# Kernel tuning notes

Measured on AMD Instinct MI355X. Metric: run time of the kernel, lower is better.

Reference implementation:

```python
import jax, jax.numpy as jnp
import numpy as np

B, S, D, H, E, K = 2, 1024, 768, 12, 8, 2
DF = 4 * D
HD = D // H
EPS = 1e-5

def layer_norm(x, g, b):
    m = jnp.mean(x, axis=-1, keepdims=True)
    v = jnp.mean(jnp.square(x - m), axis=-1, keepdims=True)
    return (x - m) * jax.lax.rsqrt(v + EPS) * g + b

def setup_inputs() -> dict:
    key = jax.random.key(0)
    ks = jax.random.split(key, 16)
    s = lambda i, shape, sc: jax.random.normal(ks[i], shape, jnp.float32) * sc
    return {
        'x': s(0, (B, S, D), 1.0),
        'ln1_g': jnp.ones((D,), jnp.float32), 'ln1_b': jnp.zeros((D,), jnp.float32),
        'Wq': s(1, (D, D), 0.02), 'Wk': s(2, (D, D), 0.02), 'Wv': s(3, (D, D), 0.02),
        'Wo': s(4, (D, D), 0.02), 'bo': jnp.zeros((D,), jnp.float32),
        'ln2_g': jnp.ones((D,), jnp.float32), 'ln2_b': jnp.zeros((D,), jnp.float32),
        'Wr': s(5, (D, E), 0.02), 'br': jnp.zeros((E,), jnp.float32),
        'W1': s(6, (E, D, DF), 0.02), 'b1': jnp.zeros((E, DF), jnp.float32),
        'W2': s(7, (E, DF, D), 0.02), 'b2': jnp.zeros((E, D), jnp.float32),
    }

def _attn(xn, Wq, Wk, Wv, Wo, bo):
    # xn: [B,S,D]
    q = (xn @ Wq).reshape(B, S, H, HD).transpose(0, 2, 1, 3)
    k = (xn @ Wk).reshape(B, S, H, HD).transpose(0, 2, 1, 3)
    v = (xn @ Wv).reshape(B, S, H, HD).transpose(0, 2, 1, 3)
    scores = jnp.einsum('bhqd,bhkd->bhqk', q, k) / jnp.sqrt(jnp.float32(HD))
    causal = jnp.tril(jnp.ones((S, S), bool))
    scores = jnp.where(causal, scores, jnp.float32(-1e9))
    w = jax.nn.softmax(scores, axis=-1)
    out = jnp.einsum('bhqk,bhkd->bhqd', w, v)
    out = out.transpose(0, 2, 1, 3).reshape(B, S, D)
    return out @ Wo + bo

def _smoe(xn, Wr, br, W1, b1, W2, b2):
    logits = xn @ Wr + br                               # [B,S,E]
    topv, topi = jax.lax.top_k(logits, K)               # [B,S,K]
    gw = jax.nn.softmax(topv, axis=-1)                  # softmax over selected experts
    oh = jax.nn.one_hot(topi, E, dtype=xn.dtype)        # [B,S,K,E]
    gate = jnp.einsum('bske,bsk->bse', oh, gw)          # sparse gate, zeros elsewhere
    h = jax.nn.gelu(jnp.einsum('bsd,edf->bsef', xn, W1) + b1, approximate=False)
    eo = jnp.einsum('bsef,efd->bsed', h, W2) + b2       # [B,S,E,D]
    return jnp.einsum('bsed,bse->bsd', eo, gate)

def reference(x, ln1_g, ln1_b, Wq, Wk, Wv, Wo, bo, ln2_g, ln2_b, Wr, br, W1, b1, W2, b2):
    h = x + _attn(layer_norm(x, ln1_g, ln1_b), Wq, Wk, Wv, Wo, bo)
    out = h + _smoe(layer_norm(h, ln2_g, ln2_b), Wr, br, W1, b1, W2, b2)
    return out
```

## Files before the change

kernel.cpp:

```cpp
#include <hip/hip_runtime.h>

using bf16x8 = __attribute__((ext_vector_type(8))) short;
using f32x4  = __attribute__((ext_vector_type(4))) float;

#define DEV __device__ __forceinline__

DEV short f2bf(float x){
  unsigned u = __float_as_uint(x);
  u += 0x7fffu + ((u >> 16) & 1u);
  return (short)(u >> 16);
}
DEV float bf2f(short h){ return __uint_as_float(((unsigned)(unsigned short)h) << 16); }

#define MFMA16(a,b,c) __builtin_amdgcn_mfma_f32_16x16x32_bf16(a,b,c,0,0,0)

DEV void gl_lds16(const void* g, void* l){
  __builtin_amdgcn_global_load_lds(
      (const __attribute__((address_space(1))) unsigned*)g,
      (__attribute__((address_space(3))) unsigned*)l, 16, 0, 0);
}


__global__ void k_transpose(const float* __restrict__ src, long sbatch,
                            short* __restrict__ dhi, short* __restrict__ dlo, long dbatch,
                            int R, int C){
  __shared__ float tile[32][33];
  const float* s = src + (long)blockIdx.z * sbatch;
  int c0 = blockIdx.x * 32, r0 = blockIdx.y * 32;
  int tx = threadIdx.x & 31, ty = threadIdx.x >> 5;
  #pragma unroll
  for (int i = 0; i < 4; i++)
    tile[ty + 8*i][tx] = s[(long)(r0 + ty + 8*i) * C + c0 + tx];
  __syncthreads();
  #pragma unroll
  for (int i = 0; i < 4; i++){
    int c = c0 + ty + 8*i;
    float v = tile[tx][ty + 8*i];
    short hv = f2bf(v);
    long o = (long)blockIdx.z * dbatch + (long)c * R + r0 + tx;
    dhi[o] = hv;
    if (dlo) dlo[o] = f2bf(v - bf2f(hv));
  }
}

__global__ void k_ln1(const float* __restrict__ x, const float* __restrict__ g,
                      const float* __restrict__ bb,
                      short* __restrict__ xh, short* __restrict__ xl){
  int t = blockIdx.x, tid = threadIdx.x;
  const float* xr = x + (long)t * 768;
  float v[3];
  #pragma unroll
  for (int j = 0; j < 3; j++) v[j] = xr[tid + 256*j];
  float s = v[0]+v[1]+v[2];
  float q = v[0]*v[0]+v[1]*v[1]+v[2]*v[2];
  #pragma unroll
  for (int o = 32; o > 0; o >>= 1){ s += __shfl_down(s,o,64); q += __shfl_down(q,o,64); }
  __shared__ float ss[4], qs[4];
  int w = tid >> 6;
  if ((tid & 63) == 0){ ss[w] = s; qs[w] = q; }
  __syncthreads();
  float St = ss[0]+ss[1]+ss[2]+ss[3], Qt = qs[0]+qs[1]+qs[2]+qs[3];
  float mean = St * (1.f/768.f);
  float var  = Qt * (1.f/768.f) - mean*mean;
  float inv  = 1.f / sqrtf(var + 1e-5f);
  #pragma unroll
  for (int j = 0; j < 3; j++){
    int d = tid + 256*j;
    float xn = (v[j]-mean)*inv*g[d] + bb[d];
    short hv = f2bf(xn);
    xh[(long)t*768 + d] = hv;
    xl[(long)t*768 + d] = f2bf(xn - bf2f(hv));
  }
}

__global__ __launch_bounds__(256,2) void k_qkv(
    const short* __restrict__ Ah, const short* __restrict__ Al,
    const short* __restrict__ Bh, const short* __restrict__ Bl,
    short* __restrict__ qh, short* __restrict__ ql,
    short* __restrict__ kh, short* __restrict__ kl,
    short* __restrict__ vh, short* __restrict__ vl){
  int M0 = blockIdx.x * 128, N0 = blockIdx.y * 128;
  __shared__ __align__(16) short lah[128*32], lal[128*32], lbh[128*32], lbl[128*32];
  int tid = threadIdx.x;
  int w = tid >> 6, lane = tid & 63, l15 = lane & 15, quad = lane >> 4;
  int mbase = (w & 1) * 64, nbase = (w >> 1) * 64;
  f32x4 acc[4][4];
  #pragma unroll
  for (int i = 0; i < 4; i++)
    #pragma unroll
    for (int j = 0; j < 4; j++) acc[i][j] = (f32x4){0.f,0.f,0.f,0.f};
  int sr = w*32 + (lane >> 2);
  int sc = ((lane & 3) ^ (sr & 3)) * 8;
  long gA = (long)(M0 + sr)*768 + sc;
  long gB = (long)(N0 + sr)*768 + sc;
  int swq = (quad ^ (l15 & 3)) * 8;
  for (int k0 = 0; k0 < 768; k0 += 32){
    gl_lds16(Ah + gA + k0,          lah + w*1024);
    gl_lds16(Ah + gA + 16*768 + k0, lah + w*1024 + 512);
    gl_lds16(Al + gA + k0,          lal + w*1024);
    gl_lds16(Al + gA + 16*768 + k0, lal + w*1024 + 512);
    gl_lds16(Bh + gB + k0,          lbh + w*1024);
    gl_lds16(Bh + gB + 16*768 + k0, lbh + w*1024 + 512);
    gl_lds16(Bl + gB + k0,          lbl + w*1024);
    gl_lds16(Bl + gB + 16*768 + k0, lbl + w*1024 + 512);
    __syncthreads();
    bf16x8 afh[4], afl[4];
    #pragma unroll
    for (int mt = 0; mt < 4; mt++){
      afh[mt] = *(const bf16x8*)&lah[(mbase+mt*16+l15)*32 + swq];
      afl[mt] = *(const bf16x8*)&lal[(mbase+mt*16+l15)*32 + swq];
    }
    #pragma unroll
    for (int nt = 0; nt < 4; nt++){
      bf16x8 bfh = *(const bf16x8*)&lbh[(nbase+nt*16+l15)*32 + swq];
      bf16x8 bfl = *(const bf16x8*)&lbl[(nbase+nt*16+l15)*32 + swq];
      #pragma unroll
      for (int mt = 0; mt < 4; mt++){
        acc[mt][nt] = MFMA16(afh[mt], bfh, acc[mt][nt]);
        acc[mt][nt] = MFMA16(afh[mt], bfl, acc[mt][nt]);
        acc[mt][nt] = MFMA16(afl[mt], bfh, acc[mt][nt]);
      }
    }
    __syncthreads();
  }
  #pragma unroll
  for (int mt = 0; mt < 4; mt++){
    #pragma unroll
    for (int nt = 0; nt < 4; nt++){
      #pragma unroll
      for (int rg = 0; rg < 4; rg++){
        int m = M0 + mbase + mt*16 + quad*4 + rg;
        int n = N0 + nbase + nt*16 + l15;
        float vv = acc[mt][nt][rg];
        int bi = m >> 10, si = m & 1023;
        if (n < 768){
          float sv = vv * 0.125f;
          short hv = f2bf(sv);
          int hh = n >> 6, hd = n & 63;
          long o = (((long)(bi*12+hh)*1024) + si)*64 + hd;
          qh[o] = hv; ql[o] = f2bf(sv - bf2f(hv));
        } else if (n < 1536){
          int n2 = n - 768;
          short hv = f2bf(vv);
          int hh = n2 >> 6, hd = n2 & 63;
          long o = (((long)(bi*12+hh)*1024) + si)*64 + hd;
          kh[o] = hv; kl[o] = f2bf(vv - bf2f(hv));
        } else {
          int n2 = n - 1536;
          short hv = f2bf(vv);
          int hh = n2 >> 6, hd = n2 & 63;
          long o = (((long)(bi*12+hh)*64) + hd)*1024 + si;
          vh[o] = hv; vl[o] = f2bf(vv - bf2f(hv));
        }
      }
    }
  }
}

__global__ __launch_bounds__(256,3) void k_attn(
    const short* __restrict__ qh, const short* __restrict__ ql,
    const short* __restrict__ kh, const short* __restrict__ kl,
    const short* __restrict__ vth, const short* __restrict__ vtl,
    float* __restrict__ po, float* __restrict__ pm, float* __restrict__ pl){
  int qt = blockIdx.x >> 1, half = blockIdx.x & 1, bh = blockIdx.y;
  int q0 = qt * 64;
  long base = (long)bh * 1024 * 64;
  int ktb = half ? ((qt + 2) >> 1) : 0;
  int kte = half ? (qt + 1) : ((qt + 2) >> 1);
  __shared__ __align__(16) short skh[64*64], skl[64*64], svh[64*64], svl[64*64];
  __shared__ __align__(16) short sph[4][16*72], spl[4][16*72];
  int tid = threadIdx.x, w = tid >> 6, lane = tid & 63, l15 = lane & 15, quad = lane >> 4;
  bf16x8 qfh[2], qfl[2];
  #pragma unroll
  for (int c = 0; c < 2; c++){
    long qa = base + (long)(q0 + w*16 + l15)*64 + c*32 + quad*8;
    qfh[c] = *(const bf16x8*)(qh + qa);
    qfl[c] = *(const bf16x8*)(ql + qa);
  }
  f32x4 oacc[4];
  #pragma unroll
  for (int i = 0; i < 4; i++) oacc[i] = (f32x4){0.f,0.f,0.f,0.f};
  float m_i[4] = {-1e30f,-1e30f,-1e30f,-1e30f};
  float l_i[4] = {0.f,0.f,0.f,0.f};
  const short* gsrc = (w==0) ? kh : (w==1) ? kl : (w==2) ? vth : vtl;
  short* myb = (w==0) ? skh : (w==1) ? skl : (w==2) ? svh : svl;
  bool isv = (w >= 2);
  int rloc = lane >> 3, pch = lane & 7;
  for (int kt = ktb; kt < kte; kt++){
    #pragma unroll
    for (int j = 0; j < 8; j++){
      int r = j*8 + rloc;
      int c = pch ^ (r & 7);
      long ga = isv ? (base + (long)r*1024 + kt*64 + c*8)
                    : (base + (long)(kt*64 + r)*64 + c*8);
      gl_lds16(gsrc + ga, myb + j*512);
    }
    __syncthreads();
    f32x4 sfr[4];
    #pragma unroll
    for (int nt = 0; nt < 4; nt++){
      f32x4 c = (f32x4){0.f,0.f,0.f,0.f};
      int krow = (nt*16 + l15) * 64;
      #pragma unroll
      for (int ch = 0; ch < 2; ch++){
        int pc = ((ch*4 + quad) ^ (l15 & 7)) * 8;
        bf16x8 kfh = *(const bf16x8*)&skh[krow + pc];
        bf16x8 kfl = *(const bf16x8*)&skl[krow + pc];
        c = MFMA16(qfh[ch], kfh, c);
        c = MFMA16(qfh[ch], kfl, c);
        c = MFMA16(qfl[ch], kfh, c);
      }
      sfr[nt] = c;
    }
    if (kt == qt){
      #pragma unroll
      for (int nt = 0; nt < 4; nt++)
        #pragma unroll
        for (int rg = 0; rg < 4; rg++){
          int kp = nt*16 + l15, qp = w*16 + quad*4 + rg;
          if (kp > qp) sfr[nt][rg] = -1e30f;
        }
    }
    float rmax[4];
    #pragma unroll
    for (int rg = 0; rg < 4; rg++)
      rmax[rg] = fmaxf(fmaxf(sfr[0][rg], sfr[1][rg]), fmaxf(sfr[2][rg], sfr[3][rg]));
    #pragma unroll
    for (int xm = 1; xm < 16; xm <<= 1)
      #pragma unroll
      for (int rg = 0; rg < 4; rg++)
        rmax[rg] = fmaxf(rmax[rg], __shfl_xor(rmax[rg], xm, 64));
    float alpha[4];
    #pragma unroll
    for (int rg = 0; rg < 4; rg++){
      float mn = fmaxf(m_i[rg], rmax[rg]);
      alpha[rg] = expf(m_i[rg] - mn);
      m_i[rg] = mn;
    }
    float rsum[4] = {0.f,0.f,0.f,0.f};
    #pragma unroll
    for (int nt = 0; nt < 4; nt++)
      #pragma unroll
      for (int rg = 0; rg < 4; rg++){
        float p = expf(sfr[nt][rg] - m_i[rg]);
        sfr[nt][rg] = p; rsum[rg] += p;
      }
    #pragma unroll
    for (int xm = 1; xm < 16; xm <<= 1)
      #pragma unroll
      for (int rg = 0; rg < 4; rg++)
        rsum[rg] += __shfl_xor(rsum[rg], xm, 64);
    #pragma unroll
    for (int rg = 0; rg < 4; rg++) l_i[rg] = l_i[rg]*alpha[rg] + rsum[rg];
    #pragma unroll
    for (int hd = 0; hd < 4; hd++)
      #pragma unroll
      for (int rg = 0; rg < 4; rg++) oacc[hd][rg] *= alpha[rg];
    #pragma unroll
    for (int nt = 0; nt < 4; nt++)
      #pragma unroll
      for (int rg = 0; rg < 4; rg++){
        float p = sfr[nt][rg];
        short hv = f2bf(p);
        sph[w][(quad*4+rg)*72 + nt*16 + l15] = hv;
        spl[w][(quad*4+rg)*72 + nt*16 + l15] = f2bf(p - bf2f(hv));
      }
    bf16x8 pfh[2], pfl[2];
    #pragma unroll
    for (int ch = 0; ch < 2; ch++){
      pfh[ch] = *(const bf16x8*)&sph[w][l15*72 + ch*32 + quad*8];
      pfl[ch] = *(const bf16x8*)&spl[w][l15*72 + ch*32 + quad*8];
    }
    #pragma unroll
    for (int hd = 0; hd < 4; hd++){
      int vrow = (hd*16 + l15) * 64;
      #pragma unroll
      for (int ch = 0; ch < 2; ch++){
        int pc = ((ch*4 + quad) ^ (l15 & 7)) * 8;
        bf16x8 vfh = *(const bf16x8*)&svh[vrow + pc];
        bf16x8 vfl = *(const bf16x8*)&svl[vrow + pc];
        oacc[hd] = MFMA16(pfh[ch], vfh, oacc[hd]);
        oacc[hd] = MFMA16(pfh[ch], vfl, oacc[hd]);
        oacc[hd] = MFMA16(pfl[ch], vfh, oacc[hd]);
      }
    }
    __syncthreads();
  }
  long pb = ((long)(half*24 + bh)*1024);
  #pragma unroll
  for (int hdt = 0; hdt < 4; hdt++)
    #pragma unroll
    for (int rg = 0; rg < 4; rg++){
      int qp = q0 + w*16 + quad*4 + rg;
      po[(pb + qp)*64 + hdt*16 + l15] = oacc[hdt][rg];
    }
  if (l15 == 0){
    #pragma unroll
    for (int rg = 0; rg < 4; rg++){
      int qp = q0 + w*16 + quad*4 + rg;
      pm[pb + qp] = m_i[rg];
      pl[pb + qp] = l_i[rg];
    }
  }
}

__global__ void k_attn_combine(const float* __restrict__ po, const float* __restrict__ pm,
                               const float* __restrict__ pl,
                               short* __restrict__ oh, short* __restrict__ ol){
  int bh = blockIdx.y, tid = threadIdx.x;
  int r = blockIdx.x*64 + (tid >> 2);
  int c0 = (tid & 3) * 16;
  long i0 = (long)bh*1024 + r;
  long i1 = (long)(24 + bh)*1024 + r;
  float m0 = pm[i0], m1 = pm[i1], l0 = pl[i0], l1 = pl[i1];
  float m = fmaxf(m0, m1);
  float a0 = expf(m0 - m), a1 = expf(m1 - m);
  float inv = 1.f / (a0*l0 + a1*l1);
  a0 *= inv; a1 *= inv;
  int b = bh / 12, hh = bh % 12;
  long ob = ((long)(b*1024 + r))*768 + hh*64 + c0;
  short hv[16], lv[16];
  #pragma unroll
  for (int j = 0; j < 4; j++){
    float4 o0 = *(const float4*)&po[i0*64 + c0 + j*4];
    float4 o1 = *(const float4*)&po[i1*64 + c0 + j*4];
    float vs[4] = {a0*o0.x + a1*o1.x, a0*o0.y + a1*o1.y,
                   a0*o0.z + a1*o1.z, a0*o0.w + a1*o1.w};
    #pragma unroll
    for (int q = 0; q < 4; q++){
      short h = f2bf(vs[q]);
      hv[j*4+q] = h; lv[j*4+q] = f2bf(vs[q] - bf2f(h));
    }
  }
  *(bf16x8*)(oh + ob)     = *(bf16x8*)&hv[0];
  *(bf16x8*)(oh + ob + 8) = *(bf16x8*)&hv[8];
  *(bf16x8*)(ol + ob)     = *(bf16x8*)&lv[0];
  *(bf16x8*)(ol + ob + 8) = *(bf16x8*)&lv[8];
}

__global__ __launch_bounds__(256,2) void k_wo(
    const short* __restrict__ Ah, const short* __restrict__ Al,
    const short* __restrict__ Bh, const short* __restrict__ Bl,
    const float* __restrict__ x, const float* __restrict__ bo,
    float* __restrict__ hout){
  int M0 = blockIdx.x * 128, N0 = blockIdx.y * 128;
  __shared__ __align__(16) short lah[128*32], lal[128*32], lbh[128*32], lbl[128*32];
  int tid = threadIdx.x;
  int w = tid >> 6, lane = tid & 63, l15 = lane & 15, quad = lane >> 4;
  int mbase = (w & 1) * 64, nbase = (w >> 1) * 64;
  f32x4 acc[4][4];
  #pragma unroll
  for (int i = 0; i < 4; i++)
    #pragma unroll
    for (int j = 0; j < 4; j++) acc[i][j] = (f32x4){0.f,0.f,0.f,0.f};
  int sr = w*32 + (lane >> 2);
  int sc = ((lane & 3) ^ (sr & 3)) * 8;
  long gA = (long)(M0 + sr)*768 + sc;
  long gB = (long)(N0 + sr)*768 + sc;
  int swq = (quad ^ (l15 & 3)) * 8;
  for (int k0 = 0; k0 < 768; k0 += 32){
    gl_lds16(Ah + gA + k0,          lah + w*1024);
    gl_lds16(Ah + gA + 16*768 + k0, lah + w*1024 + 512);
    gl_lds16(Al + gA + k0,          lal + w*1024);
    gl_lds16(Al + gA + 16*768 + k0, lal + w*1024 + 512);
    gl_lds16(Bh + gB + k0,          lbh + w*1024);
    gl_lds16(Bh + gB + 16*768 + k0, lbh + w*1024 + 512);
    gl_lds16(Bl + gB + k0,          lbl + w*1024);
    gl_lds16(Bl + gB + 16*768 + k0, lbl + w*1024 + 512);
    __syncthreads();
    bf16x8 afh[4], afl[4];
    #pragma unroll
    for (int mt = 0; mt < 4; mt++){
      afh[mt] = *(const bf16x8*)&lah[(mbase+mt*16+l15)*32 + swq];
      afl[mt] = *(const bf16x8*)&lal[(mbase+mt*16+l15)*32 + swq];
    }
    #pragma unroll
    for (int nt = 0; nt < 4; nt++){
      bf16x8 bfh = *(const bf16x8*)&lbh[(nbase+nt*16+l15)*32 + swq];
      bf16x8 bfl = *(const bf16x8*)&lbl[(nbase+nt*16+l15)*32 + swq];
      #pragma unroll
      for (int mt = 0; mt < 4; mt++){
        acc[mt][nt] = MFMA16(afh[mt], bfh, acc[mt][nt]);
        acc[mt][nt] = MFMA16(afh[mt], bfl, acc[mt][nt]);
        acc[mt][nt] = MFMA16(afl[mt], bfh, acc[mt][nt]);
      }
    }
    __syncthreads();
  }
  #pragma unroll
  for (int mt = 0; mt < 4; mt++)
    #pragma unroll
    for (int nt = 0; nt < 4; nt++)
      #pragma unroll
      for (int rg = 0; rg < 4; rg++){
        int m = M0 + mbase + mt*16 + quad*4 + rg;
        int n = N0 + nbase + nt*16 + l15;
        hout[(long)m*768 + n] = acc[mt][nt][rg] + x[(long)m*768 + n] + bo[n];
      }
}

__global__ void k_zero(int* cnt){ if (threadIdx.x < 8) cnt[threadIdx.x] = 0; }

__global__ void k_router(const float* __restrict__ h, const float* __restrict__ g,
                         const float* __restrict__ bb, const float* __restrict__ Wr,
                         const float* __restrict__ br, short* __restrict__ xn2,
                         int* __restrict__ cnt, int* __restrict__ perm,
                         float* __restrict__ gw){
  int t = blockIdx.x, tid = threadIdx.x;
  const float* xr = h + (long)t * 768;
  float v[3];
  #pragma unroll
  for (int j = 0; j < 3; j++) v[j] = xr[tid + 256*j];
  float s = v[0]+v[1]+v[2];
  float q = v[0]*v[0]+v[1]*v[1]+v[2]*v[2];
  #pragma unroll
  for (int o = 32; o > 0; o >>= 1){ s += __shfl_down(s,o,64); q += __shfl_down(q,o,64); }
  __shared__ float ss[4], qs[4];
  __shared__ float lred[4][8];
  int w = tid >> 6;
  if ((tid & 63) == 0){ ss[w] = s; qs[w] = q; }
  __syncthreads();
  float St = ss[0]+ss[1]+ss[2]+ss[3], Qt = qs[0]+qs[1]+qs[2]+qs[3];
  float mean = St * (1.f/768.f);
  float var  = Qt * (1.f/768.f) - mean*mean;
  float inv  = 1.f / sqrtf(var + 1e-5f);
  float part[8] = {0,0,0,0,0,0,0,0};
  #pragma unroll
  for (int j = 0; j < 3; j++){
    int d = tid + 256*j;
    float xn = (v[j]-mean)*inv*g[d] + bb[d];
    xn2[(long)t*768 + d] = f2bf(xn);
    #pragma unroll
    for (int e = 0; e < 8; e++) part[e] += xn * Wr[d*8 + e];
  }
  #pragma unroll
  for (int o = 32; o > 0; o >>= 1)
    #pragma unroll
    for (int e = 0; e < 8; e++) part[e] += __shfl_down(part[e], o, 64);
  if ((tid & 63) == 0)
    #pragma unroll
    for (int e = 0; e < 8; e++) lred[w][e] = part[e];
  __syncthreads();
  if (tid == 0){
    float lg[8];
    #pragma unroll
    for (int e = 0; e < 8; e++) lg[e] = lred[0][e]+lred[1][e]+lred[2][e]+lred[3][e] + br[e];
    int i1 = 0;
    for (int e = 1; e < 8; e++) if (lg[e] > lg[i1]) i1 = e;
    int i2 = -1;
    for (int e = 0; e < 8; e++){ if (e == i1) continue; if (i2 < 0 || lg[e] > lg[i2]) i2 = e; }
    float e2 = expf(lg[i2] - lg[i1]);
    float is = 1.f / (1.f + e2);
    gw[t*2]   = is;
    gw[t*2+1] = e2 * is;
    int p1 = atomicAdd(&cnt[i1], 1); perm[i1*2048 + p1] = t*2;
    int p2 = atomicAdd(&cnt[i2], 1); perm[i2*2048 + p2] = t*2 + 1;
  }
}

__global__ void k_scan(const int* __restrict__ cnt, int* __restrict__ offs){
  if (threadIdx.x == 0){
    int a = 0;
    for (int e = 0; e < 8; e++){ offs[e] = a; a += cnt[e]; }
  }
}

__global__ __launch_bounds__(256,2) void k_moe1(
    const short* __restrict__ xn2, const short* __restrict__ W1T,
    const float* __restrict__ b1,
    const int* __restrict__ cnt, const int* __restrict__ offs,
    const int* __restrict__ perm, short* __restrict__ h1){
  int e = blockIdx.x;
  int count = cnt[e];
  int M0 = blockIdx.z * 128;
  if (M0 >= count) return;
  int N0 = blockIdx.y * 128;
  const short* Bp = W1T + (long)e * 3072 * 768;
  __shared__ __align__(16) short la[128*32], lb[128*32];
  __shared__ int rtok[128];
  int tid = threadIdx.x, w = tid >> 6, lane = tid & 63, l15 = lane & 15, quad = lane >> 4;
  if (tid < 128){
    int m = M0 + tid; if (m >= count) m = count - 1;
    rtok[tid] = perm[e*2048 + m];
  }
  __syncthreads();
  int sr0 = w*32 + (lane >> 2);
  int sc  = ((lane & 3) ^ (sr0 & 3)) * 8;
  long gA0 = (long)(rtok[sr0]    >> 1)*768 + sc;
  long gA1 = (long)(rtok[sr0+16] >> 1)*768 + sc;
  long gB0 = (long)(N0 + sr0)     *768 + sc;
  long gB1 = (long)(N0 + sr0 + 16)*768 + sc;
  short* ldA = &la[w*1024];
  short* ldB = &lb[w*1024];
  f32x4 acc[4][4];
  #pragma unroll
  for (int i = 0; i < 4; i++)
    #pragma unroll
    for (int j = 0; j < 4; j++) acc[i][j] = (f32x4){0.f,0.f,0.f,0.f};
  int mbase = (w & 1) * 64, nbase = (w >> 1) * 64;
  int swq = (quad ^ (l15 & 3)) * 8;
  for (int k0 = 0; k0 < 768; k0 += 32){
    gl_lds16(xn2 + gA0 + k0, ldA);
    gl_lds16(xn2 + gA1 + k0, ldA + 512);
    gl_lds16(Bp  + gB0 + k0, ldB);
    gl_lds16(Bp  + gB1 + k0, ldB + 512);
    __syncthreads();
    bf16x8 af[4];
    #pragma unroll
    for (int mt = 0; mt < 4; mt++)
      af[mt] = *(const bf16x8*)&la[(mbase+mt*16+l15)*32 + swq];
    #pragma unroll
    for (int nt = 0; nt < 4; nt++){
      bf16x8 bf = *(const bf16x8*)&lb[(nbase+nt*16+l15)*32 + swq];
      #pragma unroll
      for (int mt = 0; mt < 4; mt++) acc[mt][nt] = MFMA16(af[mt], bf, acc[mt][nt]);
    }
    __syncthreads();
  }
  int base = offs[e];
  #pragma unroll
  for (int mt = 0; mt < 4; mt++)
    #pragma unroll
    for (int nt = 0; nt < 4; nt++)
      #pragma unroll
      for (int rg = 0; rg < 4; rg++){
        int m = M0 + mbase + mt*16 + quad*4 + rg;
        if (m < count){
          int n = N0 + nbase + nt*16 + l15;
          float vv = acc[mt][nt][rg] + b1[e*3072 + n];
          float gl = 0.5f * vv * (1.f + erff(vv * 0.70710678118654752f));
          h1[(long)(base + m)*3072 + n] = f2bf(gl);
        }
      }
}

__global__ __launch_bounds__(256,2) void k_moe2(
    const short* __restrict__ h1, const short* __restrict__ W2T,
    const float* __restrict__ b2,
    const int* __restrict__ cnt, const int* __restrict__ offs,
    const int* __restrict__ perm, const float* __restrict__ gw,
    float* __restrict__ eo){
  int e = blockIdx.x;
  int count = cnt[e];
  int M0 = blockIdx.z * 128;
  if (M0 >= count) return;
  int N0 = (blockIdx.y % 6) * 128;
  int ks = blockIdx.y / 6;
  const short* Bp = W2T + (long)e * 768 * 3072;
  int base = offs[e];
  __shared__ __align__(16) short la[128*32], lb[128*32];
  __shared__ int rtok[128];
  int tid = threadIdx.x, w = tid >> 6, lane = tid & 63, l15 = lane & 15, quad = lane >> 4;
  if (tid < 128){
    int m = M0 + tid; if (m >= count) m = count - 1;
    rtok[tid] = perm[e*2048 + m];
  }
  __syncthreads();
  int sr0 = w*32 + (lane >> 2);
  int sc  = ((lane & 3) ^ (sr0 & 3)) * 8;
  int ar0 = M0 + sr0;      if (ar0 >= count) ar0 = count - 1;
  int ar1 = M0 + sr0 + 16; if (ar1 >= count) ar1 = count - 1;
  long gA0 = (long)(base + ar0)*3072 + sc;
  long gA1 = (long)(base + ar1)*3072 + sc;
  long gB0 = (long)(N0 + sr0)     *3072 + sc;
  long gB1 = (long)(N0 + sr0 + 16)*3072 + sc;
  short* ldA = &la[w*1024];
  short* ldB = &lb[w*1024];
  f32x4 acc[4][4];
  #pragma unroll
  for (int i = 0; i < 4; i++)
    #pragma unroll
    for (int j = 0; j < 4; j++) acc[i][j] = (f32x4){0.f,0.f,0.f,0.f};
  int mbase = (w & 1) * 64, nbase = (w >> 1) * 64;
  int swq = (quad ^ (l15 & 3)) * 8;
  int kbeg = ks * 1536, kend = kbeg + 1536;
  for (int k0 = kbeg; k0 < kend; k0 += 32){
    gl_lds16(h1 + gA0 + k0, ldA);
    gl_lds16(h1 + gA1 + k0, ldA + 512);
    gl_lds16(Bp + gB0 + k0, ldB);
    gl_lds16(Bp + gB1 + k0, ldB + 512);
    __syncthreads();
    bf16x8 af[4];
    #pragma unroll
    for (int mt = 0; mt < 4; mt++)
      af[mt] = *(const bf16x8*)&la[(mbase+mt*16+l15)*32 + swq];
    #pragma unroll
    for (int nt = 0; nt < 4; nt++){
      bf16x8 bf = *(const bf16x8*)&lb[(nbase+nt*16+l15)*32 + swq];
      #pragma unroll
      for (int mt = 0; mt < 4; mt++) acc[mt][nt] = MFMA16(af[mt], bf, acc[mt][nt]);
    }
    __syncthreads();
  }
  #pragma unroll
  for (int mt = 0; mt < 4; mt++)
    #pragma unroll
    for (int nt = 0; nt < 4; nt++)
      #pragma unroll
      for (int rg = 0; rg < 4; rg++){
        int m = M0 + mbase + mt*16 + quad*4 + rg;
        if (m < count){
          int n = N0 + nbase + nt*16 + l15;
          int dv = rtok[m - M0];
          float vv = acc[mt][nt][rg] + (ks ? 0.f : b2[e*768 + n]);
          atomicAdd(&eo[(long)dv*768 + n], vv * gw[dv]);
        }
      }
}

__global__ void k_combine(const float* __restrict__ h, const float* __restrict__ eo,
                          float* __restrict__ out){
  int i = blockIdx.x * 256 + threadIdx.x;
  int t = i / 192, c = i - t * 192;
  const float4* h4 = (const float4*)h;
  const float4* e4 = (const float4*)eo;
  float4 a  = h4[i];
  float4 x0 = e4[(long)(2*t)*192 + c];
  float4 x1 = e4[(long)(2*t+1)*192 + c];
  float4 o;
  o.x = a.x + x0.x + x1.x;
  o.y = a.y + x0.y + x1.y;
  o.z = a.z + x0.z + x1.z;
  o.w = a.w + x0.w + x1.w;
  ((float4*)out)[i] = o;
}

extern "C" void kernel_launch(void* const* d_in, const int* in_sizes, int n_in,
                              void* d_out, int out_size, void* d_ws, size_t ws_size,
                              hipStream_t stream){
  const float* x    = (const float*)d_in[0];
  const float* ln1g = (const float*)d_in[1];
  const float* ln1b = (const float*)d_in[2];
  const float* Wq   = (const float*)d_in[3];
  const float* Wk   = (const float*)d_in[4];
  const float* Wv   = (const float*)d_in[5];
  const float* Wo   = (const float*)d_in[6];
  const float* bo   = (const float*)d_in[7];
  const float* ln2g = (const float*)d_in[8];
  const float* ln2b = (const float*)d_in[9];
  const float* Wr   = (const float*)d_in[10];
  const float* br   = (const float*)d_in[11];
  const float* W1   = (const float*)d_in[12];
  const float* b1   = (const float*)d_in[13];
  const float* W2   = (const float*)d_in[14];
  const float* b2   = (const float*)d_in[15];

  char* ws = (char*)d_ws;
  size_t off = 0;
  auto alloc = [&](size_t bytes) -> void* {
    void* p = ws + off;
    off += (bytes + 255) & ~(size_t)255;
    return p;
  };
  short* WQKVH = (short*)alloc(2304l*768*2);
  short* WQKVL = (short*)alloc(2304l*768*2);
  short* WOH   = (short*)alloc(768l*768*2);
  short* WOL   = (short*)alloc(768l*768*2);
  short* W1T   = (short*)alloc(8l*3072*768*2);
  short* W2T   = (short*)alloc(8l*768*3072*2);
  short* XN1H  = (short*)alloc(2048l*768*2);
  short* XN1L  = (short*)alloc(2048l*768*2);
  short* QH    = (short*)alloc(2048l*768*2);
  short* QL    = (short*)alloc(2048l*768*2);
  short* KH    = (short*)alloc(2048l*768*2);
  short* KL    = (short*)alloc(2048l*768*2);
  short* VTH   = (short*)alloc(2048l*768*2);
  short* VTL   = (short*)alloc(2048l*768*2);
  short* ATH   = (short*)alloc(2048l*768*2);
  short* ATL   = (short*)alloc(2048l*768*2);
  float* HBUF  = (float*)alloc(2048l*768*4);
  short* XN2   = (short*)alloc(2048l*768*2);
  short* H1    = (short*)alloc(4096l*3072*2);
  float* EO    = (float*)alloc(4096l*768*4);
  float* PO    = (float*)alloc(2l*24*1024*64*4);
  float* PM    = (float*)alloc(2l*24*1024*4);
  float* PL    = (float*)alloc(2l*24*1024*4);
  int*   CNT   = (int*)alloc(8*4);
  int*   OFFS  = (int*)alloc(16*4);
  int*   PERM  = (int*)alloc(8l*2048*4);
  float* GW    = (float*)alloc(4096*4);
  (void)ws_size; (void)in_sizes; (void)n_in; (void)out_size;

  k_transpose<<<dim3(24,24,1),256,0,stream>>>(Wq, 0, WQKVH,             WQKVL,             0, 768, 768);
  k_transpose<<<dim3(24,24,1),256,0,stream>>>(Wk, 0, WQKVH + 768l*768,  WQKVL + 768l*768,  0, 768, 768);
  k_transpose<<<dim3(24,24,1),256,0,stream>>>(Wv, 0, WQKVH + 1536l*768, WQKVL + 1536l*768, 0, 768, 768);
  k_transpose<<<dim3(24,24,1),256,0,stream>>>(Wo, 0, WOH, WOL, 0, 768, 768);
  k_transpose<<<dim3(96,24,8),256,0,stream>>>(W1, 768l*3072, W1T, nullptr, 3072l*768, 768, 3072);
  k_transpose<<<dim3(24,96,8),256,0,stream>>>(W2, 3072l*768, W2T, nullptr, 768l*3072, 3072, 768);

  k_ln1<<<2048,256,0,stream>>>(x, ln1g, ln1b, XN1H, XN1L);
  k_qkv<<<dim3(16,18),256,0,stream>>>(XN1H, XN1L, WQKVH, WQKVL, QH, QL, KH, KL, VTH, VTL);
  k_attn<<<dim3(32,24),256,0,stream>>>(QH, QL, KH, KL, VTH, VTL, PO, PM, PL);
  k_attn_combine<<<dim3(16,24),256,0,stream>>>(PO, PM, PL, ATH, ATL);
  k_wo<<<dim3(16,6),256,0,stream>>>(ATH, ATL, WOH, WOL, x, bo, HBUF);

  k_zero<<<1,64,0,stream>>>(CNT);
  k_router<<<2048,256,0,stream>>>(HBUF, ln2g, ln2b, Wr, br, XN2, CNT, PERM, GW);
  k_scan<<<1,64,0,stream>>>(CNT, OFFS);
  hipMemsetAsync(EO, 0, 4096l*768*4, stream);
  k_moe1<<<dim3(8,24,16),256,0,stream>>>(XN2, W1T, b1, CNT, OFFS, PERM, H1);
  k_moe2<<<dim3(8,12,16),256,0,stream>>>(H1, W2T, b2, CNT, OFFS, PERM, GW, EO);
  k_combine<<<1536,256,0,stream>>>(HBUF, EO, (float*)d_out);
}
```

Before: 530.5 us.

## Pad expert groups to 128-row tiles with a compact grid and BK=64 MoE GEMMs

Expert token groups are each padded to a multiple of 128 rows, and a block-to-expert index is built so the MoE GEMM grids launch only the tiles that exist instead of 8x16 mostly-empty blocks. A fill kernel writes a padded permutation in which padding rows are marked -1. Both MoE GEMMs now load 64-wide K slices with an 8-way XOR swizzle, which halves the number of barrier pairs. The launch bound rises to 3 blocks per CU, and moe2 is split four ways along K, which adds more atomics. The cost is extra padded rows, a larger H1 buffer and one more small kernel launch.

```diff
diff --git a/kernel.cpp b/kernel.cpp
--- a/kernel.cpp
+++ b/kernel.cpp
@@ -458,137 +458,159 @@
   }
 }
 
-__global__ void k_scan(const int* __restrict__ cnt, int* __restrict__ offs){
+__global__ void k_scan(const int* __restrict__ cnt, int* __restrict__ poffs,
+                       int* __restrict__ eidx, int* __restrict__ ptot){
   if (threadIdx.x == 0){
-    int a = 0;
-    for (int e = 0; e < 8; e++){ offs[e] = a; a += cnt[e]; }
-  }
-}
-
-__global__ __launch_bounds__(256,2) void k_moe1(
+    int p = 0;
+    for (int e = 0; e < 8; e++){
+      poffs[e] = p;
+      int pc = (cnt[e] + 127) & ~127;
+      for (int j = p >> 7; j < (p + pc) >> 7; j++) eidx[j] = e;
+      p += pc;
+    }
+    *ptot = p;
+    for (int j = p >> 7; j < 40; j++) eidx[j] = 7;
+  }
+}
+
+__global__ void k_fill(const int* __restrict__ cnt, const int* __restrict__ poffs,
+                       const int* __restrict__ eidx, const int* __restrict__ perm,
+                       const int* __restrict__ ptot, int* __restrict__ pperm){
+  int i = blockIdx.x*256 + threadIdx.x;
+  int e = eidx[i >> 7];
+  int li = i - poffs[e];
+  int v = -1;
+  if (i < *ptot && li >= 0 && li < cnt[e]) v = perm[e*2048 + li];
+  pperm[i] = v;
+}
+
+__global__ __launch_bounds__(256,3) void k_moe1(
     const short* __restrict__ xn2, const short* __restrict__ W1T,
     const float* __restrict__ b1,
-    const int* __restrict__ cnt, const int* __restrict__ offs,
-    const int* __restrict__ perm, short* __restrict__ h1){
-  int e = blockIdx.x;
-  int count = cnt[e];
-  int M0 = blockIdx.z * 128;
-  if (M0 >= count) return;
+    const int* __restrict__ eidx, const int* __restrict__ pperm,
+    const int* __restrict__ ptot, short* __restrict__ h1){
+  int Mb = blockIdx.x;
+  int M0 = Mb * 128;
+  if (M0 >= *ptot) return;
+  int e = eidx[Mb];
   int N0 = blockIdx.y * 128;
   const short* Bp = W1T + (long)e * 3072 * 768;
-  __shared__ __align__(16) short la[128*32], lb[128*32];
+  __shared__ __align__(16) short la[128*64], lb[128*64];
   __shared__ int rtok[128];
   int tid = threadIdx.x, w = tid >> 6, lane = tid & 63, l15 = lane & 15, quad = lane >> 4;
-  if (tid < 128){
-    int m = M0 + tid; if (m >= count) m = count - 1;
-    rtok[tid] = perm[e*2048 + m];
-  }
+  if (tid < 128) rtok[tid] = pperm[M0 + tid];
   __syncthreads();
-  int sr0 = w*32 + (lane >> 2);
-  int sc  = ((lane & 3) ^ (sr0 & 3)) * 8;
-  long gA0 = (long)(rtok[sr0]    >> 1)*768 + sc;
-  long gA1 = (long)(rtok[sr0+16] >> 1)*768 + sc;
-  long gB0 = (long)(N0 + sr0)     *768 + sc;
-  long gB1 = (long)(N0 + sr0 + 16)*768 + sc;
-  short* ldA = &la[w*1024];
-  short* ldB = &lb[w*1024];
+  int rl = lane >> 3, pch = lane & 7;
+  long gA[4], gB[4];
+  #pragma unroll
+  for (int j = 0; j < 4; j++){
+    int r = w*32 + j*8 + rl;
+    int c = pch ^ (r & 7);
+    int tk = rtok[r]; tk = (tk >= 0) ? (tk >> 1) : 0;
+    gA[j] = (long)tk*768 + c*8;
+    gB[j] = (long)(N0 + r)*768 + c*8;
+  }
+  short* ldA = la + w*2048;
+  short* ldB = lb + w*2048;
   f32x4 acc[4][4];
   #pragma unroll
   for (int i = 0; i < 4; i++)
     #pragma unroll
     for (int j = 0; j < 4; j++) acc[i][j] = (f32x4){0.f,0.f,0.f,0.f};
   int mbase = (w & 1) * 64, nbase = (w >> 1) * 64;
-  int swq = (quad ^ (l15 & 3)) * 8;
-  for (int k0 = 0; k0 < 768; k0 += 32){
-    gl_lds16(xn2 + gA0 + k0, ldA);
-    gl_lds16(xn2 + gA1 + k0, ldA + 512);
-    gl_lds16(Bp  + gB0 + k0, ldB);
-    gl_lds16(Bp  + gB1 + k0, ldB + 512);
-    __syncthreads();
-    bf16x8 af[4];
-    #pragma unroll
-    for (int mt = 0; mt < 4; mt++)
-      af[mt] = *(const bf16x8*)&la[(mbase+mt*16+l15)*32 + swq];
-    #pragma unroll
-    for (int nt = 0; nt < 4; nt++){
-      bf16x8 bf = *(const bf16x8*)&lb[(nbase+nt*16+l15)*32 + swq];
-      #pragma unroll
-      for (int mt = 0; mt < 4; mt++) acc[mt][nt] = MFMA16(af[mt], bf, acc[mt][nt]);
-    }
-    __syncthreads();
-  }
-  int base = offs[e];
+  for (int k0 = 0; k0 < 768; k0 += 64){
+    #pragma unroll
+    for (int j = 0; j < 4; j++) gl_lds16(xn2 + gA[j] + k0, ldA + j*512);
+    #pragma unroll
+    for (int j = 0; j < 4; j++) gl_lds16(Bp  + gB[j] + k0, ldB + j*512);
+    __syncthreads();
+    #pragma unroll
+    for (int kk = 0; kk < 2; kk++){
+      int swq = ((kk*4 + quad) ^ (l15 & 7)) * 8;
+      bf16x8 af[4];
+      #pragma unroll
+      for (int mt = 0; mt < 4; mt++)
+        af[mt] = *(const bf16x8*)&la[(mbase+mt*16+l15)*64 + swq];
+      #pragma unroll
+      for (int nt = 0; nt < 4; nt++){
+        bf16x8 bf = *(const bf16x8*)&lb[(nbase+nt*16+l15)*64 + swq];
+        #pragma unroll
+        for (int mt = 0; mt < 4; mt++) acc[mt][nt] = MFMA16(af[mt], bf, acc[mt][nt]);
+      }
+    }
+    __syncthreads();
+  }
   #pragma unroll
   for (int mt = 0; mt < 4; mt++)
     #pragma unroll
     for (int nt = 0; nt < 4; nt++)
       #pragma unroll
       for (int rg = 0; rg < 4; rg++){
-        int m = M0 + mbase + mt*16 + quad*4 + rg;
-        if (m < count){
+        int ml = mbase + mt*16 + quad*4 + rg;
+        if (rtok[ml] >= 0){
           int n = N0 + nbase + nt*16 + l15;
           float vv = acc[mt][nt][rg] + b1[e*3072 + n];
           float gl = 0.5f * vv * (1.f + erff(vv * 0.70710678118654752f));
-          h1[(long)(base + m)*3072 + n] = f2bf(gl);
+          h1[(long)(M0 + ml)*3072 + n] = f2bf(gl);
         }
       }
 }
 
-__global__ __launch_bounds__(256,2) void k_moe2(
+__global__ __launch_bounds__(256,3) void k_moe2(
     const short* __restrict__ h1, const short* __restrict__ W2T,
     const float* __restrict__ b2,
-    const int* __restrict__ cnt, const int* __restrict__ offs,
-    const int* __restrict__ perm, const float* __restrict__ gw,
+    const int* __restrict__ eidx, const int* __restrict__ pperm,
+    const int* __restrict__ ptot, const float* __restrict__ gw,
     float* __restrict__ eo){
-  int e = blockIdx.x;
-  int count = cnt[e];
-  int M0 = blockIdx.z * 128;
-  if (M0 >= count) return;
-  int N0 = (blockIdx.y % 6) * 128;
-  int ks = blockIdx.y / 6;
+  int Mb = blockIdx.x;
+  int M0 = Mb * 128;
+  if (M0 >= *ptot) return;
+  int e = eidx[Mb];
+  int N0 = blockIdx.y * 128;
+  int ks = blockIdx.z;
   const short* Bp = W2T + (long)e * 768 * 3072;
-  int base = offs[e];
-  __shared__ __align__(16) short la[128*32], lb[128*32];
+  __shared__ __align__(16) short la[128*64], lb[128*64];
   __shared__ int rtok[128];
   int tid = threadIdx.x, w = tid >> 6, lane = tid & 63, l15 = lane & 15, quad = lane >> 4;
-  if (tid < 128){
-    int m = M0 + tid; if (m >= count) m = count - 1;
-    rtok[tid] = perm[e*2048 + m];
-  }
+  if (tid < 128) rtok[tid] = pperm[M0 + tid];
   __syncthreads();
-  int sr0 = w*32 + (lane >> 2);
-  int sc  = ((lane & 3) ^ (sr0 & 3)) * 8;
-  int ar0 = M0 + sr0;      if (ar0 >= count) ar0 = count - 1;
-  int ar1 = M0 + sr0 + 16; if (ar1 >= count) ar1 = count - 1;
-  long gA0 = (long)(base + ar0)*3072 + sc;
-  long gA1 = (long)(base + ar1)*3072 + sc;
-  long gB0 = (long)(N0 + sr0)     *3072 + sc;
-  long gB1 = (long)(N0 + sr0 + 16)*3072 + sc;
-  short* ldA = &la[w*1024];
-  short* ldB = &lb[w*1024];
+  int rl = lane >> 3, pch = lane & 7;
+  int kbeg = ks * 768;
+  long gA[4], gB[4];
+  #pragma unroll
+  for (int j = 0; j < 4; j++){
+    int r = w*32 + j*8 + rl;
+    int c = pch ^ (r & 7);
+    gA[j] = (long)(M0 + r)*3072 + kbeg + c*8;
+    gB[j] = (long)(N0 + r)*3072 + kbeg + c*8;
+  }
+  short* ldA = la + w*2048;
+  short* ldB = lb + w*2048;
   f32x4 acc[4][4];
   #pragma unroll
   for (int i = 0; i < 4; i++)
     #pragma unroll
     for (int j = 0; j < 4; j++) acc[i][j] = (f32x4){0.f,0.f,0.f,0.f};
   int mbase = (w & 1) * 64, nbase = (w >> 1) * 64;
-  int swq = (quad ^ (l15 & 3)) * 8;
-  int kbeg = ks * 1536, kend = kbeg + 1536;
-  for (int k0 = kbeg; k0 < kend; k0 += 32){
-    gl_lds16(h1 + gA0 + k0, ldA);
-    gl_lds16(h1 + gA1 + k0, ldA + 512);
-    gl_lds16(Bp + gB0 + k0, ldB);
-    gl_lds16(Bp + gB1 + k0, ldB + 512);
-    __syncthreads();
-    bf16x8 af[4];
-    #pragma unroll
-    for (int mt = 0; mt < 4; mt++)
-      af[mt] = *(const bf16x8*)&la[(mbase+mt*16+l15)*32 + swq];
-    #pragma unroll
-    for (int nt = 0; nt < 4; nt++){
-      bf16x8 bf = *(const bf16x8*)&lb[(nbase+nt*16+l15)*32 + swq];
-      #pragma unroll
-      for (int mt = 0; mt < 4; mt++) acc[mt][nt] = MFMA16(af[mt], bf, acc[mt][nt]);
+  for (int k0 = 0; k0 < 768; k0 += 64){
+    #pragma unroll
+    for (int j = 0; j < 4; j++) gl_lds16(h1 + gA[j] + k0, ldA + j*512);
+    #pragma unroll
+    for (int j = 0; j < 4; j++) gl_lds16(Bp + gB[j] + k0, ldB + j*512);
+    __syncthreads();
+    #pragma unroll
+    for (int kk = 0; kk < 2; kk++){
+      int swq = ((kk*4 + quad) ^ (l15 & 7)) * 8;
+      bf16x8 af[4];
+      #pragma unroll
+      for (int mt = 0; mt < 4; mt++)
+        af[mt] = *(const bf16x8*)&la[(mbase+mt*16+l15)*64 + swq];
+      #pragma unroll
+      for (int nt = 0; nt < 4; nt++){
+        bf16x8 bf = *(const bf16x8*)&lb[(nbase+nt*16+l15)*64 + swq];
+        #pragma unroll
+        for (int mt = 0; mt < 4; mt++) acc[mt][nt] = MFMA16(af[mt], bf, acc[mt][nt]);
+      }
     }
     __syncthreads();
   }
@@ -598,10 +620,10 @@
     for (int nt = 0; nt < 4; nt++)
       #pragma unroll
       for (int rg = 0; rg < 4; rg++){
-        int m = M0 + mbase + mt*16 + quad*4 + rg;
-        if (m < count){
+        int ml = mbase + mt*16 + quad*4 + rg;
+        int dv = rtok[ml];
+        if (dv >= 0){
           int n = N0 + nbase + nt*16 + l15;
-          int dv = rtok[m - M0];
           float vv = acc[mt][nt][rg] + (ks ? 0.f : b2[e*768 + n]);
           atomicAdd(&eo[(long)dv*768 + n], vv * gw[dv]);
         }
@@ -670,14 +692,17 @@
   short* ATL   = (short*)alloc(2048l*768*2);
   float* HBUF  = (float*)alloc(2048l*768*4);
   short* XN2   = (short*)alloc(2048l*768*2);
-  short* H1    = (short*)alloc(4096l*3072*2);
+  short* H1    = (short*)alloc(5120l*3072*2);
   float* EO    = (float*)alloc(4096l*768*4);
   float* PO    = (float*)alloc(2l*24*1024*64*4);
   float* PM    = (float*)alloc(2l*24*1024*4);
   float* PL    = (float*)alloc(2l*24*1024*4);
   int*   CNT   = (int*)alloc(8*4);
-  int*   OFFS  = (int*)alloc(16*4);
+  int*   POFF  = (int*)alloc(8*4);
+  int*   EIDX  = (int*)alloc(40*4);
+  int*   PTOT  = (int*)alloc(4);
   int*   PERM  = (int*)alloc(8l*2048*4);
+  int*   PPERM = (int*)alloc(5120*4);
   float* GW    = (float*)alloc(4096*4);
   (void)ws_size; (void)in_sizes; (void)n_in; (void)out_size;
 
@@ -696,9 +721,10 @@
 
   k_zero<<<1,64,0,stream>>>(CNT);
   k_router<<<2048,256,0,stream>>>(HBUF, ln2g, ln2b, Wr, br, XN2, CNT, PERM, GW);
-  k_scan<<<1,64,0,stream>>>(CNT, OFFS);
+  k_scan<<<1,64,0,stream>>>(CNT, POFF, EIDX, PTOT);
+  k_fill<<<20,256,0,stream>>>(CNT, POFF, EIDX, PERM, PTOT, PPERM);
   hipMemsetAsync(EO, 0, 4096l*768*4, stream);
-  k_moe1<<<dim3(8,24,16),256,0,stream>>>(XN2, W1T, b1, CNT, OFFS, PERM, H1);
-  k_moe2<<<dim3(8,12,16),256,0,stream>>>(H1, W2T, b2, CNT, OFFS, PERM, GW, EO);
+  k_moe1<<<dim3(40,24),256,0,stream>>>(XN2, W1T, b1, EIDX, PPERM, PTOT, H1);
+  k_moe2<<<dim3(40,6,4),256,0,stream>>>(H1, W2T, b2, EIDX, PPERM, PTOT, GW, EO);
   k_combine<<<1536,256,0,stream>>>(HBUF, EO, (float*)d_out);
 }
```

Result: slower. 570.3 us (+7.5%).
